# Performance work log

Measured on AMD Instinct MI355X. Metric: run time of the kernel, lower is better.

Reference implementation:

```python
import jax, jax.numpy as jnp
import numpy as np

NUM_SHOT = 1024
D_MODEL = 512
NHEAD = 8
NLAYERS = 6
D_FF = 2048
EPS = 1e-5


def _ln(x, s, b):
    m = jnp.mean(x, axis=-1, keepdims=True)
    v = jnp.mean(jnp.square(x - m), axis=-1, keepdims=True)
    return (x - m) / jnp.sqrt(v + EPS) * s + b


def _mha(q_in, kv_in, w_qkv, b_qkv, w_o, b_o):
    # q_in: [Sq, D], kv_in: [Sk, D]; PyTorch in_proj layout [3D, D]
    D = q_in.shape[-1]
    hd = D // NHEAD
    wq, wk, wv = w_qkv[:D], w_qkv[D:2 * D], w_qkv[2 * D:]
    bq, bk, bv = b_qkv[:D], b_qkv[D:2 * D], b_qkv[2 * D:]
    q = (q_in @ wq.T + bq).reshape(-1, NHEAD, hd)
    k = (kv_in @ wk.T + bk).reshape(-1, NHEAD, hd)
    v = (kv_in @ wv.T + bv).reshape(-1, NHEAD, hd)
    scores = jnp.einsum('qhd,khd->hqk', q, k) * (1.0 / np.sqrt(hd))
    a = jax.nn.softmax(scores, axis=-1)
    o = jnp.einsum('hqk,khd->qhd', a, v).reshape(-1, D)
    return o @ w_o.T + b_o


def setup_inputs() -> dict:
    key = jax.random.key(0)
    ks = iter(jax.random.split(key, 40))
    L, D, F = NLAYERS, D_MODEL, D_FF
    SC = 0.05  # weight scale, keeps activations sane

    def w(shape):
        return jax.random.normal(next(ks), shape, dtype=jnp.float32) * SC

    inp = {'shot_feature': jax.random.normal(next(ks), (NUM_SHOT, D), dtype=jnp.float32)}
    inp.update(
        enc_qkv_w=w((L, 3 * D, D)), enc_qkv_b=jnp.zeros((L, 3 * D), jnp.float32),
        enc_out_w=w((L, D, D)), enc_out_b=jnp.zeros((L, D), jnp.float32),
        enc_ff1_w=w((L, F, D)), enc_ff1_b=jnp.zeros((L, F), jnp.float32),
        enc_ff2_w=w((L, D, F)), enc_ff2_b=jnp.zeros((L, D), jnp.float32),
        enc_ln1_s=jnp.ones((L, D), jnp.float32), enc_ln1_b=jnp.zeros((L, D), jnp.float32),
        enc_ln2_s=jnp.ones((L, D), jnp.float32), enc_ln2_b=jnp.zeros((L, D), jnp.float32),
        dec_sa_qkv_w=w((L, 3 * D, D)), dec_sa_qkv_b=jnp.zeros((L, 3 * D), jnp.float32),
        dec_sa_out_w=w((L, D, D)), dec_sa_out_b=jnp.zeros((L, D), jnp.float32),
        dec_ca_qkv_w=w((L, 3 * D, D)), dec_ca_qkv_b=jnp.zeros((L, 3 * D), jnp.float32),
        dec_ca_out_w=w((L, D, D)), dec_ca_out_b=jnp.zeros((L, D), jnp.float32),
        dec_ff1_w=w((L, F, D)), dec_ff1_b=jnp.zeros((L, F), jnp.float32),
        dec_ff2_w=w((L, D, F)), dec_ff2_b=jnp.zeros((L, D), jnp.float32),
        dec_ln1_s=jnp.ones((L, D), jnp.float32), dec_ln1_b=jnp.zeros((L, D), jnp.float32),
        dec_ln2_s=jnp.ones((L, D), jnp.float32), dec_ln2_b=jnp.zeros((L, D), jnp.float32),
        dec_ln3_s=jnp.ones((L, D), jnp.float32), dec_ln3_b=jnp.zeros((L, D), jnp.float32),
        enc_norm_s=jnp.ones((D,), jnp.float32), enc_norm_b=jnp.zeros((D,), jnp.float32),
        dec_norm_s=jnp.ones((D,), jnp.float32), dec_norm_b=jnp.zeros((D,), jnp.float32),
    )
    return inp


def reference(shot_feature, enc_qkv_w, enc_qkv_b, enc_out_w, enc_out_b,
              enc_ff1_w, enc_ff1_b, enc_ff2_w, enc_ff2_b,
              enc_ln1_s, enc_ln1_b, enc_ln2_s, enc_ln2_b,
              dec_sa_qkv_w, dec_sa_qkv_b, dec_sa_out_w, dec_sa_out_b,
              dec_ca_qkv_w, dec_ca_qkv_b, dec_ca_out_w, dec_ca_out_b,
              dec_ff1_w, dec_ff1_b, dec_ff2_w, dec_ff2_b,
              dec_ln1_s, dec_ln1_b, dec_ln2_s, dec_ln2_b, dec_ln3_s, dec_ln3_b,
              enc_norm_s, enc_norm_b, dec_norm_s, dec_norm_b):
    x = shot_feature.reshape(NUM_SHOT, D_MODEL)  # batch dim of 1 squeezed

    # --- encoder (post-LN, ReLU FFN, dropout=eval identity) ---
    mem = x
    for i in range(NLAYERS):
        a = _mha(mem, mem, enc_qkv_w[i], enc_qkv_b[i], enc_out_w[i], enc_out_b[i])
        mem = _ln(mem + a, enc_ln1_s[i], enc_ln1_b[i])
        f = jax.nn.relu(mem @ enc_ff1_w[i].T + enc_ff1_b[i]) @ enc_ff2_w[i].T + enc_ff2_b[i]
        mem = _ln(mem + f, enc_ln2_s[i], enc_ln2_b[i])
    mem = _ln(mem, enc_norm_s, enc_norm_b)

    # --- decoder (tgt == src, no masks, matching original usage) ---
    y = x
    for i in range(NLAYERS):
        a = _mha(y, y, dec_sa_qkv_w[i], dec_sa_qkv_b[i], dec_sa_out_w[i], dec_sa_out_b[i])
        y = _ln(y + a, dec_ln1_s[i], dec_ln1_b[i])
        a = _mha(y, mem, dec_ca_qkv_w[i], dec_ca_qkv_b[i], dec_ca_out_w[i], dec_ca_out_b[i])
        y = _ln(y + a, dec_ln2_s[i], dec_ln2_b[i])
        f = jax.nn.relu(y @ dec_ff1_w[i].T + dec_ff1_b[i]) @ dec_ff2_w[i].T + dec_ff2_b[i]
        y = _ln(y + f, dec_ln3_s[i], dec_ln3_b[i])
    attention_out = _ln(y, dec_norm_s, dec_norm_b)  # [S, D]

    # --- fused pairwise cosine similarity (replaces O(n^2) python loop) ---
    n = attention_out / jnp.linalg.norm(attention_out, axis=1, keepdims=True)
    final_result = jax.lax.stop_gradient(n @ n.T)  # .detach() in original
    return (final_result, attention_out)
```

## Files before the change

kernel.cpp:

```cpp
#include <hip/hip_runtime.h>


#define NLAY 6

typedef __attribute__((ext_vector_type(8))) short short8;
typedef __attribute__((ext_vector_type(4))) short short4v;
typedef __attribute__((ext_vector_type(4))) float f32x4;

typedef __attribute__((address_space(3))) short lds_short;
typedef __attribute__((address_space(1))) const unsigned short g_ushort;

__device__ __forceinline__ void gload16(const unsigned short* g, short* l) {
    __builtin_amdgcn_global_load_lds((g_ushort*)g, (lds_short*)l, 16, 0, 0);
}

__device__ __forceinline__ void waitvm(int n) {
    if (n == 0)      asm volatile("s_waitcnt vmcnt(0)" ::: "memory");
    else if (n == 4) asm volatile("s_waitcnt vmcnt(4)" ::: "memory");
    else             asm volatile("s_waitcnt vmcnt(8)" ::: "memory");
}

__device__ inline unsigned short f2bu(float x) {
    unsigned u = __builtin_bit_cast(unsigned, x);
    unsigned r = (u + 0x7fffu + ((u >> 16) & 1u)) >> 16;
    return (unsigned short)r;
}

struct WCvt {
    const float* src[10];
    unsigned short* dst[10];
    long cum[11];
};

__global__ __launch_bounds__(256)
void f2ball_k(WCvt wc)
{
    const long total = wc.cum[10];
    for (long c = (long)blockIdx.x * 256 + threadIdx.x; c < total;
         c += (long)gridDim.x * 256) {
        int t = 0;
        #pragma unroll
        for (int i = 1; i < 10; ++i) if (c >= wc.cum[i]) t = i;
        const long o = (c - wc.cum[t]) * 8;
        const float* s = wc.src[t];
        unsigned short* d = wc.dst[t];
        const float4 a = *(const float4*)(s + o);
        const float4 b = *(const float4*)(s + o + 4);
        short8 v;
        v[0] = (short)f2bu(a.x); v[1] = (short)f2bu(a.y);
        v[2] = (short)f2bu(a.z); v[3] = (short)f2bu(a.w);
        v[4] = (short)f2bu(b.x); v[5] = (short)f2bu(b.y);
        v[6] = (short)f2bu(b.z); v[7] = (short)f2bu(b.w);
        *(short8*)(d + o) = v;
    }
}

__global__ __launch_bounds__(256)
void f2b_k(const float* __restrict__ s, unsigned short* __restrict__ d, long n)
{
    const long stride = (long)gridDim.x * 256;
    for (long i = (long)blockIdx.x * 256 + threadIdx.x; i * 8 < n; i += stride) {
        const long o = i * 8;
        const float4 a = *(const float4*)(s + o);
        const float4 b = *(const float4*)(s + o + 4);
        short8 v;
        v[0] = (short)f2bu(a.x); v[1] = (short)f2bu(a.y);
        v[2] = (short)f2bu(a.z); v[3] = (short)f2bu(a.w);
        v[4] = (short)f2bu(b.x); v[5] = (short)f2bu(b.y);
        v[6] = (short)f2bu(b.z); v[7] = (short)f2bu(b.w);
        *(short8*)(d + o) = v;
    }
}

template<bool RELU, bool OBF16>
__global__ __launch_bounds__(256)
void gemm3_k(const unsigned short* __restrict__ A,
             const unsigned short* __restrict__ A2, int a2_col, int lda,
             const unsigned short* __restrict__ B, int ldb,
             const float* __restrict__ bias,
             void* __restrict__ Cv, int ldc, long sC,
             int K, float alpha,
             unsigned short* __restrict__ VTp, int vt_col0, int kz)
{
    __shared__ __align__(16) short As[3][4096];
    __shared__ __align__(16) short Bs[3][4096];
    const int bz = blockIdx.z;
    const int m0 = blockIdx.y * 64;
    const int n0 = blockIdx.x * 64;
    if (A2 && n0 >= a2_col) A = A2;
    A += (long)bz * kz;
    B += (long)bz * kz;
    const int tid = threadIdx.x;
    const int w  = tid >> 6;
    const int l  = tid & 63;
    const int fr = l & 15;
    const int kc = l >> 4;

    f32x4 acc[4] = {};
    const int T = K >> 6;

    auto FILL = [&](int t, int buf) {
        const int k0 = t * 64;
        #pragma unroll
        for (int it = 0; it < 2; ++it) {
            const int row = w * 16 + it * 8 + (l >> 3);
            const int sl  = ((l & 7) ^ (row & 7)) * 8;
            gload16(A + (long)(m0 + row) * lda + k0 + sl, &As[buf][(w * 16 + it * 8) * 64]);
            gload16(B + (long)(n0 + row) * ldb + k0 + sl, &Bs[buf][(w * 16 + it * 8) * 64]);
        }
    };

    FILL(0, 0);
    if (T > 1) FILL(1, 1);
    for (int t = 0; t < T; ++t) {
        waitvm(t + 1 < T ? 4 : 0);
        __builtin_amdgcn_sched_barrier(0);
        __builtin_amdgcn_s_barrier();
        if (t + 2 < T) FILL(t + 2, (t + 2) % 3);
        const int cb = t % 3;
        #pragma unroll
        for (int ks = 0; ks < 2; ++ks) {
            const int arow = w * 16 + fr;
            const short8 af = *(const short8*)&As[cb][arow * 64 + (((ks * 4 + kc) ^ (arow & 7)) * 8)];
            #pragma unroll
            for (int c = 0; c < 4; ++c) {
                const int brow = c * 16 + fr;
                const short8 bf = *(const short8*)&Bs[cb][brow * 64 + (((ks * 4 + kc) ^ (brow & 7)) * 8)];
                acc[c] = __builtin_amdgcn_mfma_f32_16x16x32_bf16(af, bf, acc[c], 0, 0, 0);
            }
        }
    }

    #pragma unroll
    for (int c = 0; c < 4; ++c) {
        const int n = n0 + c * 16 + fr;
        const float bv = bias ? bias[n] : 0.0f;
        const bool do_vt = (VTp != nullptr) && (n >= vt_col0);
        #pragma unroll
        for (int i = 0; i < 4; ++i) {
            const long m = m0 + w * 16 + kc * 4 + i;
            float v = acc[c][i] * alpha + bv;
            if (RELU) v = fmaxf(v, 0.0f);
            if (OBF16) ((unsigned short*)Cv)[bz * sC + m * ldc + n] = f2bu(v);
            else       ((float*)Cv)[bz * sC + m * ldc + n] = v;
            if (do_vt) {
                const int vc = n - vt_col0;
                VTp[(long)(vc >> 6) * 65536 + (long)(vc & 63) * 1024 + m] = f2bu(v);
            }
        }
    }
}

__global__ __launch_bounds__(128)
void attnp_k(const unsigned short* __restrict__ QKVb,
             const unsigned short* __restrict__ VT,
             const unsigned short* __restrict__ wo,
             float* __restrict__ SLABp)
{
    __shared__ __align__(16) short U[18432];
    short* Ks = U;
    short* Vs = U + 8192;
    short* Ps = U + 16384;
    const int qt = blockIdx.x;
    const int h  = blockIdx.y;
    const int tid = threadIdx.x;
    const int w  = tid >> 6;
    const int l  = tid & 63;
    const int fr = l & 15;
    const int kc = l >> 4;

    const int qrow = qt * 32 + w * 16 + fr;
    short8 qf[2];
    qf[0] = *(const short8*)(QKVb + (long)qrow * 1536 + h * 64 + kc * 8);
    qf[1] = *(const short8*)(QKVb + (long)qrow * 1536 + h * 64 + 32 + kc * 8);

    auto FILL = [&](int t, int buf) {
        const int kb = t * 64;
        #pragma unroll
        for (int it = 0; it < 4; ++it) {
            const int row = it * 16 + w * 8 + (l >> 3);
            const int sl  = ((l & 7) ^ (row & 7)) * 8;
            gload16(QKVb + (long)(kb + row) * 1536 + 512 + h * 64 + sl,
                    Ks + buf * 4096 + (it * 16 + w * 8) * 64);
            gload16(VT + (long)h * 65536 + (long)row * 1024 + kb + sl,
                    Vs + buf * 4096 + (it * 16 + w * 8) * 64);
        }
    };

    float m_i[4], l_i[4];
    f32x4 acc_o[4] = {};
    #pragma unroll
    for (int i = 0; i < 4; ++i) { m_i[i] = -1e30f; l_i[i] = 0.f; }

    short* ps = Ps + w * 1024;

    FILL(0, 0); FILL(1, 1);
    for (int t = 0; t < 16; ++t) {
        waitvm(t == 15 ? 0 : 8);
        __builtin_amdgcn_sched_barrier(0);
        __builtin_amdgcn_s_barrier();

        f32x4 sacc[4] = {};
        const int cb = t & 1;
        #pragma unroll
        for (int ks = 0; ks < 2; ++ks) {
            #pragma unroll
            for (int c = 0; c < 4; ++c) {
                const int krow = c * 16 + fr;
                const short8 kf = *(const short8*)(Ks + cb * 4096 + krow * 64 + (((ks * 4 + kc) ^ (krow & 7)) * 8));
                sacc[c] = __builtin_amdgcn_mfma_f32_16x16x32_bf16(qf[ks], kf, sacc[c], 0, 0, 0);
            }
        }

        float p[4][4];
        #pragma unroll
        for (int i = 0; i < 4; ++i) {
            float tm = fmaxf(fmaxf(sacc[0][i], sacc[1][i]), fmaxf(sacc[2][i], sacc[3][i]));
            #pragma unroll
            for (int off = 8; off; off >>= 1) tm = fmaxf(tm, __shfl_xor(tm, off));
            tm *= 0.125f;
            const float mn = fmaxf(m_i[i], tm);
            const float sc = __expf(m_i[i] - mn);
            m_i[i] = mn;
            float ts = 0.f;
            #pragma unroll
            for (int c = 0; c < 4; ++c) { p[c][i] = __expf(sacc[c][i] * 0.125f - mn); ts += p[c][i]; }
            #pragma unroll
            for (int off = 8; off; off >>= 1) ts += __shfl_xor(ts, off);
            l_i[i] = l_i[i] * sc + ts;
            #pragma unroll
            for (int c = 0; c < 4; ++c) acc_o[c][i] *= sc;
        }

        #pragma unroll
        for (int c = 0; c < 4; ++c) {
            const int col = c * 16 + fr;
            #pragma unroll
            for (int i = 0; i < 4; ++i) {
                const int row = kc * 4 + i;
                ps[row * 64 + (((col >> 3) ^ (row & 7)) * 8) + (col & 7)] = (short)f2bu(p[c][i]);
            }
        }
        short8 pf[2];
        pf[0] = *(const short8*)(ps + fr * 64 + ((kc ^ (fr & 7)) * 8));
        pf[1] = *(const short8*)(ps + fr * 64 + (((4 + kc) ^ (fr & 7)) * 8));

        #pragma unroll
        for (int ks = 0; ks < 2; ++ks) {
            #pragma unroll
            for (int c = 0; c < 4; ++c) {
                const int drow = c * 16 + fr;
                const short8 vf = *(const short8*)(Vs + cb * 4096 + drow * 64 + (((ks * 4 + kc) ^ (drow & 7)) * 8));
                acc_o[c] = __builtin_amdgcn_mfma_f32_16x16x32_bf16(pf[ks], vf, acc_o[c], 0, 0, 0);
            }
        }
        __builtin_amdgcn_s_barrier();
        if (t + 2 < 16) FILL(t + 2, (t + 2) & 1);
    }

    short* po = Ps + w * 1024;
    #pragma unroll
    for (int c = 0; c < 4; ++c) {
        const int col = c * 16 + fr;
        #pragma unroll
        for (int i = 0; i < 4; ++i) {
            const int r = kc * 4 + i;
            po[r * 64 + (((col >> 3) ^ (r & 7)) * 8) + (col & 7)] =
                (short)f2bu(acc_o[c][i] / l_i[i]);
        }
    }
    __syncthreads();

    short* Wos = U;
    float* SLABh = SLABp + (long)h * 524288;
    const int orow = qt * 32 + w * 16;

    auto WSTAGE = [&](int c8, int buf) {
        const int n0c = c8 * 64;
        #pragma unroll
        for (int it = 0; it < 4; ++it) {
            const int rb  = w * 32 + it * 8;
            const int row = rb + (l >> 3);
            const int sl  = ((l & 7) ^ (row & 7)) * 8;
            gload16(wo + (long)(n0c + row) * 512 + h * 64 + sl, Wos + buf * 4096 + rb * 64);
        }
    };

    WSTAGE(0, 0);
    for (int c8 = 0; c8 < 8; ++c8) {
        if (c8) __syncthreads();
        if (c8 + 1 < 8) WSTAGE(c8 + 1, (c8 + 1) & 1);
        waitvm(c8 + 1 < 8 ? 4 : 0);
        __builtin_amdgcn_sched_barrier(0);
        __builtin_amdgcn_s_barrier();
        const int buf = c8 & 1;
        f32x4 a2[4] = {};
        #pragma unroll
        for (int ks = 0; ks < 2; ++ks) {
            const int q = ks * 4 + kc;
            const short8 af = *(const short8*)(po + fr * 64 + ((q ^ (fr & 7)) * 8));
            #pragma unroll
            for (int ct = 0; ct < 4; ++ct) {
                const int brn = ct * 16 + fr;
                const short8 bf = *(const short8*)(Wos + buf * 4096 + brn * 64 + ((q ^ (brn & 7)) * 8));
                a2[ct] = __builtin_amdgcn_mfma_f32_16x16x32_bf16(af, bf, a2[ct], 0, 0, 0);
            }
        }
        #pragma unroll
        for (int ct = 0; ct < 4; ++ct) {
            const int n = c8 * 64 + ct * 16 + fr;
            #pragma unroll
            for (int i = 0; i < 4; ++i)
                SLABh[(long)(orow + kc * 4 + i) * 512 + n] = a2[ct][i];
        }
    }
}

template<int NSLAB>
__global__ __launch_bounds__(256)
void ln_k(const float* __restrict__ x, const float* __restrict__ slab,
          const float* __restrict__ bias,
          const float* __restrict__ s, const float* __restrict__ b,
          float* __restrict__ out, unsigned short* __restrict__ outb)
{
    const int lane = threadIdx.x & 63;
    const int row  = (blockIdx.x << 2) + (threadIdx.x >> 6);
    const float* px = x + (long)row * 512;
    float v[8];
    float sum = 0.f;
    #pragma unroll
    for (int i = 0; i < 8; ++i) {
        const int j = lane + (i << 6);
        v[i] = px[j];
        #pragma unroll
        for (int t = 0; t < NSLAB; ++t) v[i] += slab[(long)t * 524288 + (long)row * 512 + j];
        if (NSLAB > 0) v[i] += bias[j];
        sum += v[i];
    }
    #pragma unroll
    for (int off = 32; off; off >>= 1) sum += __shfl_xor(sum, off);
    const float m = sum * (1.0f / 512.0f);
    float s2 = 0.f;
    #pragma unroll
    for (int i = 0; i < 8; ++i) { const float d = v[i] - m; s2 += d * d; }
    #pragma unroll
    for (int off = 32; off; off >>= 1) s2 += __shfl_xor(s2, off);
    const float inv = rsqrtf(s2 * (1.0f / 512.0f) + 1e-5f);
    #pragma unroll
    for (int i = 0; i < 8; ++i) {
        const int j = lane + (i << 6);
        const float r = (v[i] - m) * inv * s[j] + b[j];
        out[(long)row * 512 + j] = r;
        if (outb) outb[(long)row * 512 + j] = f2bu(r);
    }
}

__global__ __launch_bounds__(256)
void lnl2_k(const float* __restrict__ x,
            const float* __restrict__ s, const float* __restrict__ b,
            float* __restrict__ out_attn, unsigned short* __restrict__ nb)
{
    const int lane = threadIdx.x & 63;
    const int row  = (blockIdx.x << 2) + (threadIdx.x >> 6);
    const float* px = x + (long)row * 512;
    float v[8];
    float sum = 0.f;
    #pragma unroll
    for (int i = 0; i < 8; ++i) { v[i] = px[lane + (i << 6)]; sum += v[i]; }
    #pragma unroll
    for (int off = 32; off; off >>= 1) sum += __shfl_xor(sum, off);
    const float m = sum * (1.0f / 512.0f);
    float s2 = 0.f;
    #pragma unroll
    for (int i = 0; i < 8; ++i) { const float d = v[i] - m; s2 += d * d; }
    #pragma unroll
    for (int off = 32; off; off >>= 1) s2 += __shfl_xor(s2, off);
    const float inv = rsqrtf(s2 * (1.0f / 512.0f) + 1e-5f);
    float nrm = 0.f;
    #pragma unroll
    for (int i = 0; i < 8; ++i) {
        const int j = lane + (i << 6);
        v[i] = (v[i] - m) * inv * s[j] + b[j];
        out_attn[(long)row * 512 + j] = v[i];
        nrm += v[i] * v[i];
    }
    #pragma unroll
    for (int off = 32; off; off >>= 1) nrm += __shfl_xor(nrm, off);
    const float rinv = rsqrtf(nrm);
    #pragma unroll
    for (int i = 0; i < 8; ++i)
        nb[(long)row * 512 + lane + (i << 6)] = f2bu(v[i] * rinv);
}

__global__ __launch_bounds__(256)
void init_k(const float* __restrict__ x, float* __restrict__ mf, float* __restrict__ yf,
            unsigned short* __restrict__ mb, unsigned short* __restrict__ yb)
{
    const long i = ((long)blockIdx.x * 256 + threadIdx.x) * 4;
    const float4 v = *(const float4*)(x + i);
    *(float4*)(mf + i) = v;
    *(float4*)(yf + i) = v;
    short4v s;
    s[0] = (short)f2bu(v.x); s[1] = (short)f2bu(v.y);
    s[2] = (short)f2bu(v.z); s[3] = (short)f2bu(v.w);
    *(short4v*)(mb + i) = s;
    *(short4v*)(yb + i) = s;
}

static void gemm3(hipStream_t st, bool relu, bool obf16,
                  const unsigned short* A, int lda,
                  const unsigned short* B, int ldb,
                  const float* bias, void* C, int ldc, long sC,
                  int M, int N, int K, float alpha, int batch,
                  unsigned short* VTp = nullptr, int vt_col0 = 0,
                  const unsigned short* A2 = nullptr, int a2_col = 0,
                  int kz = 0)
{
    dim3 g(N / 64, M / 64, batch);
    if (obf16) {
        if (relu) gemm3_k<true,  true ><<<g, 256, 0, st>>>(A, A2, a2_col, lda, B, ldb, bias, C, ldc, sC, K, alpha, VTp, vt_col0, kz);
        else      gemm3_k<false, true ><<<g, 256, 0, st>>>(A, A2, a2_col, lda, B, ldb, bias, C, ldc, sC, K, alpha, VTp, vt_col0, kz);
    } else {
        if (relu) gemm3_k<true,  false><<<g, 256, 0, st>>>(A, A2, a2_col, lda, B, ldb, bias, C, ldc, sC, K, alpha, VTp, vt_col0, kz);
        else      gemm3_k<false, false><<<g, 256, 0, st>>>(A, A2, a2_col, lda, B, ldb, bias, C, ldc, sC, K, alpha, VTp, vt_col0, kz);
    }
}

extern "C" void kernel_launch(void* const* d_in, const int* in_sizes, int n_in,
                              void* d_out, int out_size, void* d_ws, size_t ws_size,
                              hipStream_t stream)
{
    const float* x            = (const float*)d_in[0];
    const float* enc_qkv_w    = (const float*)d_in[1];
    const float* enc_qkv_b    = (const float*)d_in[2];
    const float* enc_out_w    = (const float*)d_in[3];
    const float* enc_out_b    = (const float*)d_in[4];
    const float* enc_ff1_w    = (const float*)d_in[5];
    const float* enc_ff1_b    = (const float*)d_in[6];
    const float* enc_ff2_w    = (const float*)d_in[7];
    const float* enc_ff2_b    = (const float*)d_in[8];
    const float* enc_ln1_s    = (const float*)d_in[9];
    const float* enc_ln1_b    = (const float*)d_in[10];
    const float* enc_ln2_s    = (const float*)d_in[11];
    const float* enc_ln2_b    = (const float*)d_in[12];
    const float* dec_sa_qkv_w = (const float*)d_in[13];
    const float* dec_sa_qkv_b = (const float*)d_in[14];
    const float* dec_sa_out_w = (const float*)d_in[15];
    const float* dec_sa_out_b = (const float*)d_in[16];
    const float* dec_ca_qkv_w = (const float*)d_in[17];
    const float* dec_ca_qkv_b = (const float*)d_in[18];
    const float* dec_ca_out_w = (const float*)d_in[19];
    const float* dec_ca_out_b = (const float*)d_in[20];
    const float* dec_ff1_w    = (const float*)d_in[21];
    const float* dec_ff1_b    = (const float*)d_in[22];
    const float* dec_ff2_w    = (const float*)d_in[23];
    const float* dec_ff2_b    = (const float*)d_in[24];
    const float* dec_ln1_s    = (const float*)d_in[25];
    const float* dec_ln1_b    = (const float*)d_in[26];
    const float* dec_ln2_s    = (const float*)d_in[27];
    const float* dec_ln2_b    = (const float*)d_in[28];
    const float* dec_ln3_s    = (const float*)d_in[29];
    const float* dec_ln3_b    = (const float*)d_in[30];
    const float* enc_norm_s   = (const float*)d_in[31];
    const float* enc_norm_b   = (const float*)d_in[32];
    const float* dec_norm_s   = (const float*)d_in[33];
    const float* dec_norm_b   = (const float*)d_in[34];

    char* p = (char*)d_ws;
    auto alloc = [&](size_t bytes) -> char* {
        char* r = p; p += (bytes + 255) & ~(size_t)255; return r;
    };
    float*          MEMf = (float*)alloc(1024 * 512 * 4);
    float*          Yf   = (float*)alloc(1024 * 512 * 4);
    unsigned short* MEMb = (unsigned short*)alloc(1024 * 512 * 2);
    unsigned short* Yb   = (unsigned short*)alloc(1024 * 512 * 2);
    unsigned short* QKVb = (unsigned short*)alloc(1024 * 1536 * 2);
    unsigned short* VT   = (unsigned short*)alloc(8L * 64 * 1024 * 2);
    float*          SLAB = (float*)alloc(8L * 1024 * 512 * 4);
    unsigned short* F1b  = (unsigned short*)alloc(1024L * 2048 * 2);
    unsigned short* NBb  = (unsigned short*)alloc(1024 * 512 * 2);

    const float* wsrc[10] = {enc_qkv_w, enc_out_w, enc_ff1_w, enc_ff2_w,
                             dec_sa_qkv_w, dec_sa_out_w, dec_ca_qkv_w, dec_ca_out_w,
                             dec_ff1_w, dec_ff2_w};
    const long wper[10] = {1536L*512, 512L*512, 2048L*512, 512L*2048,
                           1536L*512, 512L*512, 1536L*512, 512L*512,
                           2048L*512, 512L*2048};
    long wtot = 0;
    for (int t = 0; t < 10; ++t) wtot += wper[t] * NLAY;

    const size_t used = (size_t)(p - (char*)d_ws);
    const bool preconv = (ws_size > used) && ((ws_size - used) >= (size_t)wtot * 2 + 4096);

    unsigned short* wpre[10] = {};
    unsigned short* slots[2] = {};
    int slot_ctr = 0;
    if (preconv) {
        WCvt wc;
        wc.cum[0] = 0;
        for (int t = 0; t < 10; ++t) {
            wpre[t] = (unsigned short*)alloc((size_t)wper[t] * NLAY * 2);
            wc.src[t] = wsrc[t];
            wc.dst[t] = wpre[t];
            wc.cum[t + 1] = wc.cum[t] + wper[t] * NLAY / 8;
        }
        f2ball_k<<<dim3(2048), 256, 0, stream>>>(wc);
    } else {
        slots[0] = (unsigned short*)alloc(2048L * 512 * 2);
        slots[1] = (unsigned short*)alloc(2048L * 512 * 2);
    }
    auto W = [&](int t, int layer) -> const unsigned short* {
        if (preconv) return wpre[t] + (long)layer * wper[t];
        unsigned short* dst = slots[(slot_ctr++) & 1];
        const long n = wper[t];
        long blocks = (n / 8 + 255) / 256; if (blocks > 2048) blocks = 2048;
        f2b_k<<<dim3((unsigned)blocks), 256, 0, stream>>>(wsrc[t] + (long)layer * wper[t], dst, n);
        return dst;
    };

    float* out_gram = (float*)d_out;
    float* out_attn = out_gram + 1024 * 1024;

    auto run_attn = [&](const unsigned short* qb, const unsigned short* kvb,
                        int wt_qkv, int wt_o, int layer, const float* bqkv,
                        const float* obias, const float* lns, const float* lnb,
                        float* xf, unsigned short* xb) {
        gemm3(stream, false, true, qb, 512, W(wt_qkv, layer), 512, bqkv,
              QKVb, 1536, 0, 1024, 1536, 512, 1.0f, 1, VT, 1024,
              (qb == kvb) ? nullptr : kvb, 512);
        attnp_k<<<dim3(32, 8), 128, 0, stream>>>(QKVb, VT, W(wt_o, layer), SLAB);
        ln_k<8><<<256, 256, 0, stream>>>(xf, SLAB, obias, lns, lnb, xf, xb);
    };
    auto run_ffn = [&](unsigned short* inb, int wt1, int wt2, int layer,
                       const float* b1, const float* f2bias,
                       const float* lns, const float* lnb,
                       float* xf, unsigned short* xb) {
        gemm3(stream, true, true, inb, 512, W(wt1, layer), 512, b1,
              F1b, 2048, 0, 1024, 2048, 512, 1.0f, 1);
        gemm3(stream, false, false, F1b, 2048, W(wt2, layer), 2048, nullptr,
              SLAB, 512, 524288, 1024, 512, 512, 1.0f, 4, nullptr, 0, nullptr, 0, 512);
        ln_k<4><<<256, 256, 0, stream>>>(xf, SLAB, f2bias, lns, lnb, xf, xb);
    };

    init_k<<<512, 256, 0, stream>>>(x, MEMf, Yf, MEMb, Yb);

    for (int i = 0; i < NLAY; ++i) {
        run_attn(MEMb, MEMb, 0, 1, i, enc_qkv_b + i * 1536,
                 enc_out_b + i * 512, enc_ln1_s + i * 512, enc_ln1_b + i * 512, MEMf, MEMb);
        run_ffn(MEMb, 2, 3, i, enc_ff1_b + i * 2048, enc_ff2_b + i * 512,
                enc_ln2_s + i * 512, enc_ln2_b + i * 512, MEMf, MEMb);
    }
    ln_k<0><<<256, 256, 0, stream>>>(MEMf, nullptr, nullptr, enc_norm_s, enc_norm_b, MEMf, MEMb);

    for (int i = 0; i < NLAY; ++i) {
        run_attn(Yb, Yb, 4, 5, i, dec_sa_qkv_b + i * 1536,
                 dec_sa_out_b + i * 512, dec_ln1_s + i * 512, dec_ln1_b + i * 512, Yf, Yb);
        run_attn(Yb, MEMb, 6, 7, i, dec_ca_qkv_b + i * 1536,
                 dec_ca_out_b + i * 512, dec_ln2_s + i * 512, dec_ln2_b + i * 512, Yf, Yb);
        run_ffn(Yb, 8, 9, i, dec_ff1_b + i * 2048, dec_ff2_b + i * 512,
                dec_ln3_s + i * 512, dec_ln3_b + i * 512, Yf, Yb);
    }

    lnl2_k<<<256, 256, 0, stream>>>(Yf, dec_norm_s, dec_norm_b, out_attn, NBb);
    gemm3(stream, false, false, NBb, 512, NBb, 512, nullptr,
          out_gram, 1024, 0, 1024, 1024, 512, 1.0f, 1);
}
```

Before: 1.170 ms.

## Use 128x64 GEMM tiles, bf16 attention partial slabs, and a dedicated Gram GEMM

The general GEMM becomes a 128x64-tile kernel in which each wave computes a 32x64 sub-tile. Loading A and B fragments once per k-step and reusing them across more MFMAs is meant to improve operand reuse. The per-head output-projection partials written by the attention kernel are now stored as bf16 instead of fp32, halving the slab traffic that the LayerNorm kernel reads back. The final Gram matrix uses a stripped-down 64x64 GEMM with no epilogue options. Costs: the bigger tiles halve the number of blocks per GEMM, which may underfill the GPU, and summing 8 bf16-rounded partials loses some precision.

Result: slower. 1.244 ms (+6.4%).

```diff
diff --git a/kernel.cpp b/kernel.cpp
--- a/kernel.cpp
+++ b/kernel.cpp
@@ -17,6 +17,7 @@
 __device__ __forceinline__ void waitvm(int n) {
     if (n == 0)      asm volatile("s_waitcnt vmcnt(0)" ::: "memory");
     else if (n == 4) asm volatile("s_waitcnt vmcnt(4)" ::: "memory");
+    else if (n == 6) asm volatile("s_waitcnt vmcnt(6)" ::: "memory");
     else             asm volatile("s_waitcnt vmcnt(8)" ::: "memory");
 }
 
@@ -24,6 +25,10 @@
     unsigned u = __builtin_bit_cast(unsigned, x);
     unsigned r = (u + 0x7fffu + ((u >> 16) & 1u)) >> 16;
     return (unsigned short)r;
+}
+
+__device__ inline float b2f(unsigned short u) {
+    return __builtin_bit_cast(float, (unsigned)u << 16);
 }
 
 struct WCvt {
@@ -74,7 +79,7 @@
 
 template<bool RELU, bool OBF16>
 __global__ __launch_bounds__(256)
-void gemm3_k(const unsigned short* __restrict__ A,
+void gemmT_k(const unsigned short* __restrict__ A,
              const unsigned short* __restrict__ A2, int a2_col, int lda,
              const unsigned short* __restrict__ B, int ldb,
              const float* __restrict__ bias,
@@ -82,10 +87,10 @@
              int K, float alpha,
              unsigned short* __restrict__ VTp, int vt_col0, int kz)
 {
-    __shared__ __align__(16) short As[3][4096];
-    __shared__ __align__(16) short Bs[3][4096];
+    __shared__ __align__(16) short As[3][128 * 64];
+    __shared__ __align__(16) short Bs[3][64 * 64];
     const int bz = blockIdx.z;
-    const int m0 = blockIdx.y * 64;
+    const int m0 = blockIdx.y * 128;
     const int n0 = blockIdx.x * 64;
     if (A2 && n0 >= a2_col) A = A2;
     A += (long)bz * kz;
@@ -96,6 +101,91 @@
     const int fr = l & 15;
     const int kc = l >> 4;
 
+    f32x4 acc[2][4] = {};
+    const int T = K >> 6;
+
+    auto FILL = [&](int t, int buf) {
+        const int k0 = t * 64;
+        #pragma unroll
+        for (int it = 0; it < 4; ++it) {
+            const int row = w * 32 + it * 8 + (l >> 3);
+            const int sl  = ((l & 7) ^ (row & 7)) * 8;
+            gload16(A + (long)(m0 + row) * lda + k0 + sl,
+                    &As[buf][(w * 32 + it * 8) * 64]);
+        }
+        #pragma unroll
+        for (int it = 0; it < 2; ++it) {
+            const int row = w * 16 + it * 8 + (l >> 3);
+            const int sl  = ((l & 7) ^ (row & 7)) * 8;
+            gload16(B + (long)(n0 + row) * ldb + k0 + sl,
+                    &Bs[buf][(w * 16 + it * 8) * 64]);
+        }
+    };
+
+    FILL(0, 0);
+    if (T > 1) FILL(1, 1);
+    for (int t = 0; t < T; ++t) {
+        waitvm(t + 1 < T ? 6 : 0);
+        __builtin_amdgcn_sched_barrier(0);
+        __builtin_amdgcn_s_barrier();
+        if (t + 2 < T) FILL(t + 2, (t + 2) % 3);
+        const int cb = t % 3;
+        #pragma unroll
+        for (int ks = 0; ks < 2; ++ks) {
+            const int sl = ((ks * 4 + kc) ^ (fr & 7)) * 8;
+            short8 af[2], bf[4];
+            #pragma unroll
+            for (int r = 0; r < 2; ++r)
+                af[r] = *(const short8*)&As[cb][(w * 32 + r * 16 + fr) * 64 + sl];
+            #pragma unroll
+            for (int c = 0; c < 4; ++c)
+                bf[c] = *(const short8*)&Bs[cb][(c * 16 + fr) * 64 + sl];
+            #pragma unroll
+            for (int r = 0; r < 2; ++r)
+                #pragma unroll
+                for (int c = 0; c < 4; ++c)
+                    acc[r][c] = __builtin_amdgcn_mfma_f32_16x16x32_bf16(af[r], bf[c], acc[r][c], 0, 0, 0);
+        }
+    }
+
+    #pragma unroll
+    for (int c = 0; c < 4; ++c) {
+        const int n = n0 + c * 16 + fr;
+        const float bv = bias ? bias[n] : 0.0f;
+        const bool do_vt = (VTp != nullptr) && (n >= vt_col0);
+        #pragma unroll
+        for (int r = 0; r < 2; ++r) {
+            #pragma unroll
+            for (int i = 0; i < 4; ++i) {
+                const long m = m0 + w * 32 + r * 16 + kc * 4 + i;
+                float v = acc[r][c][i] * alpha + bv;
+                if (RELU) v = fmaxf(v, 0.0f);
+                if (OBF16) ((unsigned short*)Cv)[bz * sC + m * ldc + n] = f2bu(v);
+                else       ((float*)Cv)[bz * sC + m * ldc + n] = v;
+                if (do_vt) {
+                    const int vc = n - vt_col0;
+                    VTp[(long)(vc >> 6) * 65536 + (long)(vc & 63) * 1024 + m] = f2bu(v);
+                }
+            }
+        }
+    }
+}
+
+__global__ __launch_bounds__(256)
+void gemm3_k(const unsigned short* __restrict__ A, int lda,
+             const unsigned short* __restrict__ B, int ldb,
+             float* __restrict__ C, int ldc, int K)
+{
+    __shared__ __align__(16) short As[3][4096];
+    __shared__ __align__(16) short Bs[3][4096];
+    const int m0 = blockIdx.y * 64;
+    const int n0 = blockIdx.x * 64;
+    const int tid = threadIdx.x;
+    const int w  = tid >> 6;
+    const int l  = tid & 63;
+    const int fr = l & 15;
+    const int kc = l >> 4;
+
     f32x4 acc[4] = {};
     const int T = K >> 6;
 
@@ -134,19 +224,10 @@
     #pragma unroll
     for (int c = 0; c < 4; ++c) {
         const int n = n0 + c * 16 + fr;
-        const float bv = bias ? bias[n] : 0.0f;
-        const bool do_vt = (VTp != nullptr) && (n >= vt_col0);
         #pragma unroll
         for (int i = 0; i < 4; ++i) {
             const long m = m0 + w * 16 + kc * 4 + i;
-            float v = acc[c][i] * alpha + bv;
-            if (RELU) v = fmaxf(v, 0.0f);
-            if (OBF16) ((unsigned short*)Cv)[bz * sC + m * ldc + n] = f2bu(v);
-            else       ((float*)Cv)[bz * sC + m * ldc + n] = v;
-            if (do_vt) {
-                const int vc = n - vt_col0;
-                VTp[(long)(vc >> 6) * 65536 + (long)(vc & 63) * 1024 + m] = f2bu(v);
-            }
+            C[m * ldc + n] = acc[c][i];
         }
     }
 }
@@ -155,7 +236,7 @@
 void attnp_k(const unsigned short* __restrict__ QKVb,
              const unsigned short* __restrict__ VT,
              const unsigned short* __restrict__ wo,
-             float* __restrict__ SLABp)
+             unsigned short* __restrict__ SLABb)
 {
     __shared__ __align__(16) short U[18432];
     short* Ks = U;
@@ -272,7 +353,7 @@
     __syncthreads();
 
     short* Wos = U;
-    float* SLABh = SLABp + (long)h * 524288;
+    unsigned short* SLABh = SLABb + (long)h * 524288;
     const int orow = qt * 32 + w * 16;
 
     auto WSTAGE = [&](int c8, int buf) {
@@ -311,14 +392,14 @@
             const int n = c8 * 64 + ct * 16 + fr;
             #pragma unroll
             for (int i = 0; i < 4; ++i)
-                SLABh[(long)(orow + kc * 4 + i) * 512 + n] = a2[ct][i];
-        }
-    }
-}
-
-template<int NSLAB>
+                SLABh[(long)(orow + kc * 4 + i) * 512 + n] = f2bu(a2[ct][i]);
+        }
+    }
+}
+
+template<int NSLAB, bool SB16>
 __global__ __launch_bounds__(256)
-void ln_k(const float* __restrict__ x, const float* __restrict__ slab,
+void ln_k(const float* __restrict__ x, const void* __restrict__ slab,
           const float* __restrict__ bias,
           const float* __restrict__ s, const float* __restrict__ b,
           float* __restrict__ out, unsigned short* __restrict__ outb)
@@ -333,7 +414,10 @@
         const int j = lane + (i << 6);
         v[i] = px[j];
         #pragma unroll
-        for (int t = 0; t < NSLAB; ++t) v[i] += slab[(long)t * 524288 + (long)row * 512 + j];
+        for (int t = 0; t < NSLAB; ++t) {
+            if (SB16) v[i] += b2f(((const unsigned short*)slab)[(long)t * 524288 + (long)row * 512 + j]);
+            else      v[i] += ((const float*)slab)[(long)t * 524288 + (long)row * 512 + j];
+        }
         if (NSLAB > 0) v[i] += bias[j];
         sum += v[i];
     }
@@ -407,7 +491,7 @@
     *(short4v*)(yb + i) = s;
 }
 
-static void gemm3(hipStream_t st, bool relu, bool obf16,
+static void gemmT(hipStream_t st, bool relu, bool obf16,
                   const unsigned short* A, int lda,
                   const unsigned short* B, int ldb,
                   const float* bias, void* C, int ldc, long sC,
@@ -416,13 +500,13 @@
                   const unsigned short* A2 = nullptr, int a2_col = 0,
                   int kz = 0)
 {
-    dim3 g(N / 64, M / 64, batch);
+    dim3 g(N / 64, M / 128, batch);
     if (obf16) {
-        if (relu) gemm3_k<true,  true ><<<g, 256, 0, st>>>(A, A2, a2_col, lda, B, ldb, bias, C, ldc, sC, K, alpha, VTp, vt_col0, kz);
-        else      gemm3_k<false, true ><<<g, 256, 0, st>>>(A, A2, a2_col, lda, B, ldb, bias, C, ldc, sC, K, alpha, VTp, vt_col0, kz);
+        if (relu) gemmT_k<true,  true ><<<g, 256, 0, st>>>(A, A2, a2_col, lda, B, ldb, bias, C, ldc, sC, K, alpha, VTp, vt_col0, kz);
+        else      gemmT_k<false, true ><<<g, 256, 0, st>>>(A, A2, a2_col, lda, B, ldb, bias, C, ldc, sC, K, alpha, VTp, vt_col0, kz);
     } else {
-        if (relu) gemm3_k<true,  false><<<g, 256, 0, st>>>(A, A2, a2_col, lda, B, ldb, bias, C, ldc, sC, K, alpha, VTp, vt_col0, kz);
-        else      gemm3_k<false, false><<<g, 256, 0, st>>>(A, A2, a2_col, lda, B, ldb, bias, C, ldc, sC, K, alpha, VTp, vt_col0, kz);
+        if (relu) gemmT_k<true,  false><<<g, 256, 0, st>>>(A, A2, a2_col, lda, B, ldb, bias, C, ldc, sC, K, alpha, VTp, vt_col0, kz);
+        else      gemmT_k<false, false><<<g, 256, 0, st>>>(A, A2, a2_col, lda, B, ldb, bias, C, ldc, sC, K, alpha, VTp, vt_col0, kz);
     }
 }
 
@@ -476,7 +560,7 @@
     unsigned short* Yb   = (unsigned short*)alloc(1024 * 512 * 2);
     unsigned short* QKVb = (unsigned short*)alloc(1024 * 1536 * 2);
     unsigned short* VT   = (unsigned short*)alloc(8L * 64 * 1024 * 2);
-    float*          SLAB = (float*)alloc(8L * 1024 * 512 * 4);
+    char*           SLAB = alloc(8L * 1024 * 512 * 2);
     unsigned short* F1b  = (unsigned short*)alloc(1024L * 2048 * 2);
     unsigned short* NBb  = (unsigned short*)alloc(1024 * 512 * 2);
 
@@ -525,21 +609,22 @@
                         int wt_qkv, int wt_o, int layer, const float* bqkv,
                         const float* obias, const float* lns, const float* lnb,
                         float* xf, unsigned short* xb) {
-        gemm3(stream, false, true, qb, 512, W(wt_qkv, layer), 512, bqkv,
+        gemmT(stream, false, true, qb, 512, W(wt_qkv, layer), 512, bqkv,
               QKVb, 1536, 0, 1024, 1536, 512, 1.0f, 1, VT, 1024,
               (qb == kvb) ? nullptr : kvb, 512);
-        attnp_k<<<dim3(32, 8), 128, 0, stream>>>(QKVb, VT, W(wt_o, layer), SLAB);
-        ln_k<8><<<256, 256, 0, stream>>>(xf, SLAB, obias, lns, lnb, xf, xb);
+        attnp_k<<<dim3(32, 8), 128, 0, stream>>>(QKVb, VT, W(wt_o, layer),
+                                                 (unsigned short*)SLAB);
+        ln_k<8, true><<<256, 256, 0, stream>>>(xf, SLAB, obias, lns, lnb, xf, xb);
     };
     auto run_ffn = [&](unsigned short* inb, int wt1, int wt2, int layer,
                        const float* b1, const float* f2bias,
                        const float* lns, const float* lnb,
                        float* xf, unsigned short* xb) {
-        gemm3(stream, true, true, inb, 512, W(wt1, layer), 512, b1,
+        gemmT(stream, true, true, inb, 512, W(wt1, layer), 512, b1,
               F1b, 2048, 0, 1024, 2048, 512, 1.0f, 1);
-        gemm3(stream, false, false, F1b, 2048, W(wt2, layer), 2048, nullptr,
+        gemmT(stream, false, false, F1b, 2048, W(wt2, layer), 2048, nullptr,
               SLAB, 512, 524288, 1024, 512, 512, 1.0f, 4, nullptr, 0, nullptr, 0, 512);
-        ln_k<4><<<256, 256, 0, stream>>>(xf, SLAB, f2bias, lns, lnb, xf, xb);
+        ln_k<4, false><<<256, 256, 0, stream>>>(xf, SLAB, f2bias, lns, lnb, xf, xb);
     };
 
     init_k<<<512, 256, 0, stream>>>(x, MEMf, Yf, MEMb, Yb);
@@ -550,7 +635,7 @@
         run_ffn(MEMb, 2, 3, i, enc_ff1_b + i * 2048, enc_ff2_b + i * 512,
                 enc_ln2_s + i * 512, enc_ln2_b + i * 512, MEMf, MEMb);
     }
-    ln_k<0><<<256, 256, 0, stream>>>(MEMf, nullptr, nullptr, enc_norm_s, enc_norm_b, MEMf, MEMb);
+    ln_k<0, false><<<256, 256, 0, stream>>>(MEMf, nullptr, nullptr, enc_norm_s, enc_norm_b, MEMf, MEMb);
 
     for (int i = 0; i < NLAY; ++i) {
         run_attn(Yb, Yb, 4, 5, i, dec_sa_qkv_b + i * 1536,
@@ -562,6 +647,5 @@
     }
 
     lnl2_k<<<256, 256, 0, stream>>>(Yf, dec_norm_s, dec_norm_b, out_attn, NBb);
-    gemm3(stream, false, false, NBb, 512, NBb, 512, nullptr,
-          out_gram, 1024, 0, 1024, 1024, 512, 1.0f, 1);
-}
+    gemm3_k<<<dim3(16, 16), 256, 0, stream>>>(NBb, 512, NBb, 512, out_gram, 1024, 512);
+}
```
